# Kernel tuning notes

Measured on AMD Instinct MI355X. Metric: run time of the kernel, lower is better.

## Reference

```python
import jax, jax.numpy as jnp
import numpy as np

GRID_SIZE = 16
KH = KW = 3


def setup_inputs() -> dict:
    key = jax.random.key(0)
    k1, k2, k3, k4 = jax.random.split(key, 4)
    B, H, W, C, F = 8, 32, 32, 64, 64
    x = jax.random.normal(k1, (B, H, W, C), dtype=jnp.float32)
    control_points = jax.random.normal(k2, (F, C, KH, KW, GRID_SIZE), dtype=jnp.float32) * 0.1
    w1 = jax.random.normal(k3, (F, C, KH, KW), dtype=jnp.float32) * 0.1
    w2 = jax.random.normal(k4, (F, C, KH, KW), dtype=jnp.float32) * 0.1
    return {"x": x, "control_points": control_points, "w1": w1, "w2": w2}


def _extract_patches_same(x, kh, kw):
    # x: (B,H,W,C), stride 1, TF 'SAME' padding -> (B,H,W,kh,kw,C)
    B, H, W, C = x.shape
    ph, pw = kh - 1, kw - 1
    xp = jnp.pad(x, ((0, 0), (ph // 2, ph - ph // 2), (pw // 2, pw - pw // 2), (0, 0)))
    taps = [xp[:, i:i + H, j:j + W, :] for i in range(kh) for j in range(kw)]
    return jnp.stack(taps, axis=3).reshape(B, H, W, kh, kw, C)


def reference(x, control_points, w1, w2):
    F, C, kh, kw, G = control_points.shape
    grid = jnp.linspace(-1.0, 1.0, G)
    patches = _extract_patches_same(x, kh, kw)  # (B,H,W,kh,kw,C)
    # spline: searchsorted + clip + linear interp on the fixed uniform grid
    xc = jnp.clip(patches, -1.0, 1.0)
    idx = jnp.clip(jnp.searchsorted(grid, xc, side='left') - 1, 0, G - 2)
    frac = (xc - grid[idx]) / (grid[idx + 1] - grid[idx])  # (B,H,W,kh,kw,C)
    # two-nonzero linear basis over control points -> (B,H,W,kh,kw,C,G)
    basis = (jax.nn.one_hot(idx, G, dtype=x.dtype) * (1.0 - frac)[..., None]
             + jax.nn.one_hot(idx + 1, G, dtype=x.dtype) * frac[..., None])
    # fuse w1 into control points, contract taps+channels+grid in one einsum
    wcp = w1[..., None] * control_points  # (F,C,kh,kw,G)
    out = jnp.einsum('bpqijcg,fcijg->bpqf', basis, wcp)
    out = out + jnp.einsum('bpqijc,fcij->bpqf', jax.nn.silu(patches), w2)
    return out  # (B,H,W,F)
```

## Files before the change

### kernel.cpp

```cpp
#include <hip/hip_runtime.h>


typedef _Float16 v8h __attribute__((ext_vector_type(8)));
typedef float    v4f __attribute__((ext_vector_type(4)));

#define NSLOT8  81920
#define NOUT4   131072

__global__ __launch_bounds__(256) void prep_wsw(const float* __restrict__ cp,
                                                const float* __restrict__ w1,
                                                const float* __restrict__ w2,
                                                _Float16* __restrict__ wsw,
                                                float* __restrict__ out) {
    int tid = blockIdx.x * 256 + threadIdx.x;
    if (tid < NSLOT8) {
        int lane = tid & 63;
        int rest = tid >> 6;
        int nt   = rest & 3;
        int ks   = rest >> 2;
        int kb   = ks * 32 + ((lane >> 4) << 3);
        int f    = (nt << 4) + (lane & 15);
        int chunk = kb / 640;
        int klb   = kb - chunk * 640;
        v8h o;
        if (klb < 576) {
            int c  = (chunk << 2) + klb / 144;
            int rb = klb % 144;
            int ij = rb >> 4;
            float w = w1[f * 576 + c * 9 + ij];
            const v4f* cpp = (const v4f*)(cp + (size_t)f * 9216 + c * 144 + rb);
            v4f lo = cpp[0], hi = cpp[1];
#pragma unroll
            for (int j = 0; j < 4; ++j) {
                o[j]     = (_Float16)(w * lo[j]);
                o[j + 4] = (_Float16)(w * hi[j]);
            }
        } else {
            int i2 = klb - 576;
            int c  = (chunk << 2) + (i2 >> 4);
            if ((i2 & 15) == 0) {
#pragma unroll
                for (int j = 0; j < 8; ++j)
                    o[j] = (_Float16)w2[f * 576 + c * 9 + j];
            } else {
#pragma unroll
                for (int j = 0; j < 8; ++j) o[j] = (_Float16)0.f;
                o[0] = (_Float16)w2[f * 576 + c * 9 + 8];
            }
        }
        ((v8h*)wsw)[tid] = o;
    }
    if (tid < NOUT4) ((v4f*)out)[tid] = (v4f){0.f, 0.f, 0.f, 0.f};
}

__global__ __launch_bounds__(256, 2) void kan_mfma(const float* __restrict__ x,
                                                   const _Float16* __restrict__ wsw,
                                                   float* __restrict__ out) {
    __shared__ __align__(16) char smem[81920];
    float* red = (float*)smem;

    int blk = blockIdx.x;
    int kh  = blk >> 7;
    int mt  = blk & 127;
    int b = mt >> 4, p0 = (mt & 15) << 1;
    int t = threadIdx.x, wv = t >> 6, lane = t & 63;
    int m = lane & 15, kq = lane >> 4;

    int ch0 = kh * 4, ch1 = ch0 + 4;
    const float* xb = x + (size_t)b * 65536;

    int xoff[3], sbase[3], smask[3], ijb[3];
    bool act[3];
#pragma unroll
    for (int it = 0; it < 3; ++it) {
        bool a = (it < 2) || (lane < 16);
        int e  = a ? (wv * 144 + it * 64 + lane) : 0;
        int q  = e / 9;
        int ij = e - q * 9;
        int di = ij / 3;
        int dj = ij - di * 3;
        int row = p0 + (q >> 5) + di - 1;
        int col = (q & 31) + dj - 1;
        bool ok = ((unsigned)row < 32u) && ((unsigned)col < 32u) && a;
        act[it]   = a;
        xoff[it]  = ok ? (row * 32 + col) * 64 : -1;
        sbase[it] = q * 1280;
        smask[it] = (q & 7) << 4;
        ijb[it]   = ij * 32;
    }

    v4f z4 = (v4f){0.f, 0.f, 0.f, 0.f};
    v4f acc[4][4];
#pragma unroll
    for (int i = 0; i < 4; ++i)
#pragma unroll
        for (int n = 0; n < 4; ++n) acc[i][n] = z4;

    for (int i4 = t; i4 < 5120; i4 += 256) ((v4f*)smem)[i4] = z4;

    v4f vbuf[3];
#pragma unroll
    for (int it = 0; it < 3; ++it)
        vbuf[it] = (xoff[it] >= 0) ? *(const v4f*)(xb + xoff[it] + ch0 * 4) : z4;
    unsigned pk[3] = {0u, 0u, 0u};

    __syncthreads();

    for (int gch = ch0; gch < ch1; ++gch) {
#pragma unroll
        for (int it = 0; it < 3; ++it) {
            if (act[it]) {
                v4f xv = vbuf[it];
                char* rowp = smem + sbase[it];
                int mask = smask[it];
                int jb   = ijb[it];
                unsigned pp = pk[it], np = 0;
#pragma unroll
                for (int cl = 0; cl < 4; ++cl) {
                    float v  = xv[cl];
                    float xc = fminf(fmaxf(v, -1.f), 1.f);
                    float tt = (xc + 1.f) * 7.5f;
                    int idx  = (int)tt;
                    if (idx > 14) idx = 14;
                    float fr = tt - (float)idx;
                    float sv = v * __builtin_amdgcn_rcpf(1.f + __expf(-v));
                    int sb0 = cl * 288 + jb;
                    if (gch > ch0) {
                        int pb = sb0 + (int)((pp >> (cl * 8)) & 255) * 2;
                        *(_Float16*)(rowp + (pb ^ mask))       = (_Float16)0.f;
                        *(_Float16*)(rowp + ((pb + 2) ^ mask)) = (_Float16)0.f;
                    }
                    int wb = sb0 + idx * 2;
                    *(_Float16*)(rowp + (wb ^ mask))       = (_Float16)(1.f - fr);
                    *(_Float16*)(rowp + ((wb + 2) ^ mask)) = (_Float16)fr;
                    *(_Float16*)(rowp + ((1152 + cl * 32 + (jb >> 4)) ^ mask))
                        = (_Float16)sv;
                    np |= (unsigned)idx << (cl * 8);
                }
                pk[it] = np;
            }
        }
        __syncthreads();
        if (gch + 1 < ch1) {
#pragma unroll
            for (int it = 0; it < 3; ++it)
                vbuf[it] = (xoff[it] >= 0)
                         ? *(const v4f*)(xb + xoff[it] + (gch + 1) * 4) : z4;
        }
        const v8h* bp = (const v8h*)wsw + ((size_t)gch * 20 + wv * 5) * 256 + lane;
        int mbase = m * 1280;
        int mm    = (m & 7) << 4;
#pragma unroll
        for (int s = 0; s < 5; ++s) {
            int kx = (((wv * 5 + s) * 64) + (kq * 16)) ^ mm;
            v8h a0 = *(const v8h*)(smem + mbase + kx);
            v8h a1 = *(const v8h*)(smem + mbase + 20480 + kx);
            v8h a2 = *(const v8h*)(smem + mbase + 40960 + kx);
            v8h a3 = *(const v8h*)(smem + mbase + 61440 + kx);
            v8h b0 = bp[s * 256];
            v8h b1 = bp[s * 256 + 64];
            v8h b2 = bp[s * 256 + 128];
            v8h b3 = bp[s * 256 + 192];
            acc[0][0] = __builtin_amdgcn_mfma_f32_16x16x32_f16(a0, b0, acc[0][0], 0, 0, 0);
            acc[0][1] = __builtin_amdgcn_mfma_f32_16x16x32_f16(a0, b1, acc[0][1], 0, 0, 0);
            acc[0][2] = __builtin_amdgcn_mfma_f32_16x16x32_f16(a0, b2, acc[0][2], 0, 0, 0);
            acc[0][3] = __builtin_amdgcn_mfma_f32_16x16x32_f16(a0, b3, acc[0][3], 0, 0, 0);
            acc[1][0] = __builtin_amdgcn_mfma_f32_16x16x32_f16(a1, b0, acc[1][0], 0, 0, 0);
            acc[1][1] = __builtin_amdgcn_mfma_f32_16x16x32_f16(a1, b1, acc[1][1], 0, 0, 0);
            acc[1][2] = __builtin_amdgcn_mfma_f32_16x16x32_f16(a1, b2, acc[1][2], 0, 0, 0);
            acc[1][3] = __builtin_amdgcn_mfma_f32_16x16x32_f16(a1, b3, acc[1][3], 0, 0, 0);
            acc[2][0] = __builtin_amdgcn_mfma_f32_16x16x32_f16(a2, b0, acc[2][0], 0, 0, 0);
            acc[2][1] = __builtin_amdgcn_mfma_f32_16x16x32_f16(a2, b1, acc[2][1], 0, 0, 0);
            acc[2][2] = __builtin_amdgcn_mfma_f32_16x16x32_f16(a2, b2, acc[2][2], 0, 0, 0);
            acc[2][3] = __builtin_amdgcn_mfma_f32_16x16x32_f16(a2, b3, acc[2][3], 0, 0, 0);
            acc[3][0] = __builtin_amdgcn_mfma_f32_16x16x32_f16(a3, b0, acc[3][0], 0, 0, 0);
            acc[3][1] = __builtin_amdgcn_mfma_f32_16x16x32_f16(a3, b1, acc[3][1], 0, 0, 0);
            acc[3][2] = __builtin_amdgcn_mfma_f32_16x16x32_f16(a3, b2, acc[3][2], 0, 0, 0);
            acc[3][3] = __builtin_amdgcn_mfma_f32_16x16x32_f16(a3, b3, acc[3][3], 0, 0, 0);
        }
        __syncthreads();
    }

#pragma unroll
    for (int mtile = 0; mtile < 4; ++mtile)
#pragma unroll
        for (int nt = 0; nt < 4; ++nt)
#pragma unroll
            for (int r = 0; r < 4; ++r)
                red[wv * 4160 + (mtile * 16 + kq * 4 + r) * 65 + nt * 16 + m]
                    = acc[mtile][nt][r];
    __syncthreads();
    int f = t & 63, pxg = t >> 6;
    float* op = out + ((size_t)(b * 32 + p0) * 32) * 64 + f;
#pragma unroll
    for (int i = 0; i < 16; ++i) {
        int px = pxg * 16 + i;
        float s = red[px * 65 + f] + red[4160 + px * 65 + f]
                + red[8320 + px * 65 + f] + red[12480 + px * 65 + f];
        atomicAdd(op + px * 64, s);
    }
}

extern "C" void kernel_launch(void* const* d_in, const int* in_sizes, int n_in,
                              void* d_out, int out_size, void* d_ws, size_t ws_size,
                              hipStream_t stream) {
    const float* x  = (const float*)d_in[0];
    const float* cp = (const float*)d_in[1];
    const float* w1 = (const float*)d_in[2];
    const float* w2 = (const float*)d_in[3];
    _Float16* wsw = (_Float16*)d_ws;
    float*    outp = (float*)d_out;

    prep_wsw<<<512, 256, 0, stream>>>(cp, w1, w2, wsw, outp);
    kan_mfma<<<512, 256, 0, stream>>>(x, wsw, outp);
}
```

Before: 86.53 us.

## Split each wave's N tiles across two waves, doubling block to 512 threads

```diff
diff --git a/kernel.cpp b/kernel.cpp
--- a/kernel.cpp
+++ b/kernel.cpp
@@ -53,7 +53,7 @@
     if (tid < NOUT4) ((v4f*)out)[tid] = (v4f){0.f, 0.f, 0.f, 0.f};
 }
 
-__global__ __launch_bounds__(256, 2) void kan_mfma(const float* __restrict__ x,
+__global__ __launch_bounds__(512, 4) void kan_mfma(const float* __restrict__ x,
                                                    const _Float16* __restrict__ wsw,
                                                    float* __restrict__ out) {
     __shared__ __align__(16) char smem[81920];
@@ -65,16 +65,17 @@
     int b = mt >> 4, p0 = (mt & 15) << 1;
     int t = threadIdx.x, wv = t >> 6, lane = t & 63;
     int m = lane & 15, kq = lane >> 4;
+    int wg = wv >> 1, nh = wv & 1;
 
     int ch0 = kh * 4, ch1 = ch0 + 4;
     const float* xb = x + (size_t)b * 65536;
 
-    int xoff[3], sbase[3], smask[3], ijb[3];
-    bool act[3];
-#pragma unroll
-    for (int it = 0; it < 3; ++it) {
-        bool a = (it < 2) || (lane < 16);
-        int e  = a ? (wv * 144 + it * 64 + lane) : 0;
+    int xoff[2], sbase[2], smask[2], ijb[2];
+    bool act[2];
+#pragma unroll
+    for (int it = 0; it < 2; ++it) {
+        bool a = (it == 0) || (lane < 8);
+        int e  = a ? (wv * 72 + it * 64 + lane) : 0;
         int q  = e / 9;
         int ij = e - q * 9;
         int di = ij / 3;
@@ -90,25 +91,25 @@
     }
 
     v4f z4 = (v4f){0.f, 0.f, 0.f, 0.f};
-    v4f acc[4][4];
+    v4f acc[4][2];
 #pragma unroll
     for (int i = 0; i < 4; ++i)
 #pragma unroll
-        for (int n = 0; n < 4; ++n) acc[i][n] = z4;
-
-    for (int i4 = t; i4 < 5120; i4 += 256) ((v4f*)smem)[i4] = z4;
-
-    v4f vbuf[3];
-#pragma unroll
-    for (int it = 0; it < 3; ++it)
+        for (int n = 0; n < 2; ++n) acc[i][n] = z4;
+
+    for (int i4 = t; i4 < 5120; i4 += 512) ((v4f*)smem)[i4] = z4;
+
+    v4f vbuf[2];
+#pragma unroll
+    for (int it = 0; it < 2; ++it)
         vbuf[it] = (xoff[it] >= 0) ? *(const v4f*)(xb + xoff[it] + ch0 * 4) : z4;
-    unsigned pk[3] = {0u, 0u, 0u};
+    unsigned pk[2] = {0u, 0u};
 
     __syncthreads();
 
     for (int gch = ch0; gch < ch1; ++gch) {
 #pragma unroll
-        for (int it = 0; it < 3; ++it) {
+        for (int it = 0; it < 2; ++it) {
             if (act[it]) {
                 v4f xv = vbuf[it];
                 char* rowp = smem + sbase[it];
@@ -143,40 +144,31 @@
         __syncthreads();
         if (gch + 1 < ch1) {
 #pragma unroll
-            for (int it = 0; it < 3; ++it)
+            for (int it = 0; it < 2; ++it)
                 vbuf[it] = (xoff[it] >= 0)
                          ? *(const v4f*)(xb + xoff[it] + (gch + 1) * 4) : z4;
         }
-        const v8h* bp = (const v8h*)wsw + ((size_t)gch * 20 + wv * 5) * 256 + lane;
+        const v8h* bp = (const v8h*)wsw
+                      + ((size_t)gch * 20 + wg * 5) * 256 + nh * 128 + lane;
         int mbase = m * 1280;
         int mm    = (m & 7) << 4;
 #pragma unroll
         for (int s = 0; s < 5; ++s) {
-            int kx = (((wv * 5 + s) * 64) + (kq * 16)) ^ mm;
+            int kx = (((wg * 5 + s) * 64) + (kq * 16)) ^ mm;
             v8h a0 = *(const v8h*)(smem + mbase + kx);
             v8h a1 = *(const v8h*)(smem + mbase + 20480 + kx);
             v8h a2 = *(const v8h*)(smem + mbase + 40960 + kx);
             v8h a3 = *(const v8h*)(smem + mbase + 61440 + kx);
             v8h b0 = bp[s * 256];
             v8h b1 = bp[s * 256 + 64];
-            v8h b2 = bp[s * 256 + 128];
-            v8h b3 = bp[s * 256 + 192];
             acc[0][0] = __builtin_amdgcn_mfma_f32_16x16x32_f16(a0, b0, acc[0][0], 0, 0, 0);
             acc[0][1] = __builtin_amdgcn_mfma_f32_16x16x32_f16(a0, b1, acc[0][1], 0, 0, 0);
-            acc[0][2] = __builtin_amdgcn_mfma_f32_16x16x32_f16(a0, b2, acc[0][2], 0, 0, 0);
-            acc[0][3] = __builtin_amdgcn_mfma_f32_16x16x32_f16(a0, b3, acc[0][3], 0, 0, 0);
             acc[1][0] = __builtin_amdgcn_mfma_f32_16x16x32_f16(a1, b0, acc[1][0], 0, 0, 0);
             acc[1][1] = __builtin_amdgcn_mfma_f32_16x16x32_f16(a1, b1, acc[1][1], 0, 0, 0);
-            acc[1][2] = __builtin_amdgcn_mfma_f32_16x16x32_f16(a1, b2, acc[1][2], 0, 0, 0);
-            acc[1][3] = __builtin_amdgcn_mfma_f32_16x16x32_f16(a1, b3, acc[1][3], 0, 0, 0);
             acc[2][0] = __builtin_amdgcn_mfma_f32_16x16x32_f16(a2, b0, acc[2][0], 0, 0, 0);
             acc[2][1] = __builtin_amdgcn_mfma_f32_16x16x32_f16(a2, b1, acc[2][1], 0, 0, 0);
-            acc[2][2] = __builtin_amdgcn_mfma_f32_16x16x32_f16(a2, b2, acc[2][2], 0, 0, 0);
-            acc[2][3] = __builtin_amdgcn_mfma_f32_16x16x32_f16(a2, b3, acc[2][3], 0, 0, 0);
             acc[3][0] = __builtin_amdgcn_mfma_f32_16x16x32_f16(a3, b0, acc[3][0], 0, 0, 0);
             acc[3][1] = __builtin_amdgcn_mfma_f32_16x16x32_f16(a3, b1, acc[3][1], 0, 0, 0);
-            acc[3][2] = __builtin_amdgcn_mfma_f32_16x16x32_f16(a3, b2, acc[3][2], 0, 0, 0);
-            acc[3][3] = __builtin_amdgcn_mfma_f32_16x16x32_f16(a3, b3, acc[3][3], 0, 0, 0);
         }
         __syncthreads();
     }
@@ -184,17 +176,17 @@
 #pragma unroll
     for (int mtile = 0; mtile < 4; ++mtile)
 #pragma unroll
-        for (int nt = 0; nt < 4; ++nt)
+        for (int ntl = 0; ntl < 2; ++ntl)
 #pragma unroll
             for (int r = 0; r < 4; ++r)
-                red[wv * 4160 + (mtile * 16 + kq * 4 + r) * 65 + nt * 16 + m]
-                    = acc[mtile][nt][r];
+                red[wg * 4160 + (mtile * 16 + kq * 4 + r) * 65
+                    + (nh * 2 + ntl) * 16 + m] = acc[mtile][ntl][r];
     __syncthreads();
-    int f = t & 63, pxg = t >> 6;
+    int f = t & 63, pg = t >> 6;
     float* op = out + ((size_t)(b * 32 + p0) * 32) * 64 + f;
 #pragma unroll
-    for (int i = 0; i < 16; ++i) {
-        int px = pxg * 16 + i;
+    for (int i = 0; i < 8; ++i) {
+        int px = pg * 8 + i;
         float s = red[px * 65 + f] + red[4160 + px * 65 + f]
                 + red[8320 + px * 65 + f] + red[12480 + px * 65 + f];
         atomicAdd(op + px * 64, s);
@@ -212,5 +204,5 @@
     float*    outp = (float*)d_out;
 
     prep_wsw<<<512, 256, 0, stream>>>(cp, w1, w2, wsw, outp);
-    kan_mfma<<<512, 256, 0, stream>>>(x, wsw, outp);
+    kan_mfma<<<512, 512, 0, stream>>>(x, wsw, outp);
 }
```

New measurement: 83.96 us. 3.0% less time.
